# Kernel optimization log

Hardware: AMD Instinct MI355X
Metric: run time of the kernel (lower is better)

The kernel has to match this reference:

```python
import math
import jax, jax.numpy as jnp
import numpy as np

B, S, D, H, DH = 2, 2048, 2048, 16, 128  # batch, seq (= n_ctx), d_model, n_heads, d_head


def _alibi_slopes(n):
    def pow2(m):
        start = 2 ** (-2 ** (-(math.log2(m) - 3)))
        return [start * start ** i for i in range(m)]
    if math.log2(n).is_integer():
        return pow2(n)
    c = 2 ** math.floor(math.log2(n))
    return pow2(c) + _alibi_slopes(2 * c)[0::2][: n - c]


def _alibi_mask(n_heads, q_len, kv_len):
    # faithful to _gen_alibi_mask: causal -inf upper triangle + slope * key_position
    slopes = jnp.asarray(np.array(_alibi_slopes(n_heads), dtype=np.float32))  # [H]
    bias = slopes[:, None, None] * jnp.arange(kv_len, dtype=jnp.float32)[None, None, :]  # [H,1,kv]
    i = jnp.arange(q_len)[:, None]
    j = jnp.arange(kv_len)[None, :]
    causal = jnp.where(j > i, -jnp.inf, 0.0).astype(jnp.float32)  # [q,kv] (q_len == kv_len here)
    return causal[None, :, :] + bias  # [H,q,kv]


def setup_inputs() -> dict:
    key = jax.random.key(0)
    k1, k2, k3, k4, k5 = jax.random.split(key, 5)
    scale = 1.0 / math.sqrt(D)
    return {
        "resid_pre": jax.random.normal(k1, (B, S, D), dtype=jnp.float32),
        "Wq": jax.random.normal(k2, (H * DH, D), dtype=jnp.float32) * scale,
        "Wk": jax.random.normal(k3, (H * DH, D), dtype=jnp.float32) * scale,
        "Wv": jax.random.normal(k4, (H * DH, D), dtype=jnp.float32) * scale,
        "Wo": jax.random.normal(k5, (D, H * DH), dtype=jnp.float32) * scale,
    }


def reference(resid_pre, Wq, Wk, Wv, Wo):
    b, s, d = resid_pre.shape
    # nn.Linear(no bias): y = x @ W^T ; view to [b, s, H, DH]
    q = (resid_pre @ Wq.T).reshape(b, s, H, DH)
    k = (resid_pre @ Wk.T).reshape(b, s, H, DH)
    v = (resid_pre @ Wv.T).reshape(b, s, H, DH)
    # QK^T / sqrt(d_head), clamp, add ALiBi+causal mask
    scores = jnp.einsum('bqhd,bkhd->bhqk', q, k) / math.sqrt(DH)
    scores = jnp.clip(scores, -1024.0, 1024.0)
    scores = scores + _alibi_mask(H, s, s)[None]  # broadcast over batch
    attn = jax.nn.softmax(scores.astype(jnp.float32), axis=-1).astype(q.dtype)
    z = jnp.einsum('bhqk,bkhd->bqhd', attn, v)  # [b,s,H,DH]
    # out_proj.weight [D, H*DH] reshaped to [D, H, DH]; per-head out summed over heads
    out = jnp.einsum('bqhd,ohd->bqo', z, Wo.reshape(d, H, DH))
    return out
```

## Files before the change

kernel.cpp:

```cpp
#include <hip/hip_runtime.h>
#include <hip/hip_bf16.h>

typedef __attribute__((ext_vector_type(4))) float f32x4;
typedef __attribute__((ext_vector_type(8))) short bf16x8;
typedef __attribute__((ext_vector_type(4))) short short4v;

__device__ __forceinline__ short f2bf(float f) {
  union { float f; unsigned u; } x; x.f = f;
  unsigned r = x.u + 0x7fffu + ((x.u >> 16) & 1u);
  return (short)(r >> 16);
}

__device__ __forceinline__ float fexp2(float x) {
#if __has_builtin(__builtin_amdgcn_exp2f)
  return __builtin_amdgcn_exp2f(x);
#else
  return exp2f(x);
#endif
}

#define WAITVM4() { asm volatile("s_waitcnt vmcnt(4)" ::: "memory"); __builtin_amdgcn_sched_barrier(0); }
#define BARRIER() { __builtin_amdgcn_sched_barrier(0); asm volatile("s_barrier" ::: "memory"); __builtin_amdgcn_sched_barrier(0); }
#define GLD16(g, l) __builtin_amdgcn_global_load_lds((const __attribute__((address_space(1))) void*)(g), (__attribute__((address_space(3))) void*)(l), 16, 0, 0)

__global__ __launch_bounds__(256) void cast_kernel(const float* __restrict__ in,
                                                   short* __restrict__ out, int n4) {
  int i = blockIdx.x * 256 + threadIdx.x;
  if (i < n4) {
    const float4 v = reinterpret_cast<const float4*>(in)[i];
    short4v s;
    s.x = f2bf(v.x); s.y = f2bf(v.y); s.z = f2bf(v.z); s.w = f2bf(v.w);
    reinterpret_cast<short4v*>(out)[i] = s;
  }
}

__global__ __launch_bounds__(256) void cast_w_kernel(const float* __restrict__ w0,
                                                     const float* __restrict__ w1,
                                                     const float* __restrict__ w2,
                                                     const float* __restrict__ w3,
                                                     short* __restrict__ qkv,
                                                     short* __restrict__ wo) {
  const int y = blockIdx.y;
  const float* in = (y == 0) ? w0 : (y == 1) ? w1 : (y == 2) ? w2 : w3;
  short* out = (y < 3) ? (qkv + (long)y * 4194304) : wo;
  const int i = blockIdx.x * 256 + threadIdx.x;
  const float4 v = reinterpret_cast<const float4*>(in)[i];
  short4v s;
  s.x = f2bf(v.x); s.y = f2bf(v.y); s.z = f2bf(v.z); s.w = f2bf(v.w);
  reinterpret_cast<short4v*>(out)[i] = s;
}

__global__ __launch_bounds__(512, 2) void gemm_qkv8(const short* __restrict__ A,
                                                    const short* __restrict__ W,
                                                    short* __restrict__ Qo,
                                                    short* __restrict__ Ko,
                                                    short* __restrict__ Vt) {
  __shared__ __align__(1024) char lds[131072];
  const int tid  = threadIdx.x;
  const int lane = tid & 63;
  const int w    = tid >> 6;
  const int wm   = w >> 2, wn = w & 3;
  const int l16  = lane & 15, g = lane >> 4;
  const int K    = 2048;

  int id = (int)blockIdx.x;
  id = (id & 7) * 48 + (id >> 3);
  const int mb = id & 15, nb = id >> 4;
  const long m0 = (long)mb * 256, n0 = (long)nb * 256;

  const int srow = lane >> 3;
  const int scol = ((lane & 7) ^ srow) * 8;
  const int csw  = (l16 & 7) << 4;

  f32x4 acc[8][4];
  #pragma unroll
  for (int a = 0; a < 8; a++)
    #pragma unroll
    for (int b = 0; b < 4; b++) acc[a][b] = (f32x4){0.f, 0.f, 0.f, 0.f};

  #define STAGE_HALF(mat, rbase, h, kt, buf, isB)                                   \
    {                                                                               \
      const long rowg = (rbase) + (h) * 128 + w * 16 + srow;                        \
      const short* s0_ = (mat) + rowg * K + (kt) * 64 + scol;                       \
      char* d_ = lds + (buf) * 65536 + (isB) * 32768 + ((h) * 128 + w * 16) * 128;  \
      GLD16(s0_, d_);                                                               \
      GLD16(s0_ + 8LL * K, d_ + 1024);                                              \
    }

  #define RDA(buf, h, fmL, k) (*reinterpret_cast<const bf16x8*>(                    \
      lds + (buf) * 65536 + (((h) * 128 + wm * 64 + (fmL) * 16 + l16) * 128) +      \
      (((k) * 64 + g * 16) ^ csw)))
  #define RDB(buf, h, fnL, k) (*reinterpret_cast<const bf16x8*>(                    \
      lds + (buf) * 65536 + 32768 + (((h) * 128 + wn * 32 + (fnL) * 16 + l16) * 128) + \
      (((k) * 64 + g * 16) ^ csw)))

  STAGE_HALF(A, m0, 0, 0, 0, 0);
  STAGE_HALF(W, n0, 0, 0, 0, 1);
  STAGE_HALF(W, n0, 1, 0, 0, 1);
  STAGE_HALF(A, m0, 1, 0, 0, 0);
  WAITVM4();
  BARRIER();

  bf16x8 af[4][2], bfr[2][2];
  for (int kt = 0; kt < 32; ++kt) {
    const int cur = kt & 1, nxt = cur ^ 1;
    const int ks = (kt + 1 < 32) ? (kt + 1) : kt;

    #pragma unroll
    for (int fm = 0; fm < 4; fm++)
      #pragma unroll
      for (int k = 0; k < 2; k++) af[fm][k] = RDA(cur, 0, fm, k);
    #pragma unroll
    for (int j = 0; j < 2; j++)
      #pragma unroll
      for (int k = 0; k < 2; k++) bfr[j][k] = RDB(cur, 0, j, k);
    STAGE_HALF(A, m0, 0, ks, nxt, 0);
    WAITVM4();
    BARRIER();
    __builtin_amdgcn_s_setprio(1);
    #pragma unroll
    for (int fm = 0; fm < 4; fm++)
      #pragma unroll
      for (int j = 0; j < 2; j++)
        #pragma unroll
        for (int k = 0; k < 2; k++)
          acc[fm][j] = __builtin_amdgcn_mfma_f32_16x16x32_bf16(af[fm][k], bfr[j][k], acc[fm][j], 0, 0, 0);
    __builtin_amdgcn_s_setprio(0);
    BARRIER();

    #pragma unroll
    for (int j = 0; j < 2; j++)
      #pragma unroll
      for (int k = 0; k < 2; k++) bfr[j][k] = RDB(cur, 1, j, k);
    STAGE_HALF(W, n0, 0, ks, nxt, 1);
    WAITVM4();
    BARRIER();
    __builtin_amdgcn_s_setprio(1);
    #pragma unroll
    for (int fm = 0; fm < 4; fm++)
      #pragma unroll
      for (int j = 0; j < 2; j++)
        #pragma unroll
        for (int k = 0; k < 2; k++)
          acc[fm][2 + j] = __builtin_amdgcn_mfma_f32_16x16x32_bf16(af[fm][k], bfr[j][k], acc[fm][2 + j], 0, 0, 0);
    __builtin_amdgcn_s_setprio(0);
    BARRIER();

    #pragma unroll
    for (int fm = 0; fm < 4; fm++)
      #pragma unroll
      for (int k = 0; k < 2; k++) af[fm][k] = RDA(cur, 1, fm, k);
    STAGE_HALF(W, n0, 1, ks, nxt, 1);
    WAITVM4();
    BARRIER();
    __builtin_amdgcn_s_setprio(1);
    #pragma unroll
    for (int fm = 0; fm < 4; fm++)
      #pragma unroll
      for (int j = 0; j < 2; j++)
        #pragma unroll
        for (int k = 0; k < 2; k++)
          acc[4 + fm][2 + j] = __builtin_amdgcn_mfma_f32_16x16x32_bf16(af[fm][k], bfr[j][k], acc[4 + fm][2 + j], 0, 0, 0);
    __builtin_amdgcn_s_setprio(0);
    BARRIER();

    #pragma unroll
    for (int j = 0; j < 2; j++)
      #pragma unroll
      for (int k = 0; k < 2; k++) bfr[j][k] = RDB(cur, 0, j, k);
    STAGE_HALF(A, m0, 1, ks, nxt, 0);
    WAITVM4();
    BARRIER();
    __builtin_amdgcn_s_setprio(1);
    #pragma unroll
    for (int fm = 0; fm < 4; fm++)
      #pragma unroll
      for (int j = 0; j < 2; j++)
        #pragma unroll
        for (int k = 0; k < 2; k++)
          acc[4 + fm][j] = __builtin_amdgcn_mfma_f32_16x16x32_bf16(af[fm][k], bfr[j][k], acc[4 + fm][j], 0, 0, 0);
    __builtin_amdgcn_s_setprio(0);
    BARRIER();
  }

  const int sect = (int)(n0 >> 11);
  #pragma unroll
  for (int fm = 0; fm < 8; fm++)
    #pragma unroll
    for (int fn = 0; fn < 4; fn++) {
      const long row0 = m0 + (fm >> 2) * 128 + wm * 64 + (fm & 3) * 16 + g * 4;
      const long col  = n0 + (fn >> 1) * 128 + wn * 32 + (fn & 1) * 16 + l16;
      if (sect == 0) {
        #pragma unroll
        for (int i = 0; i < 4; i++) Qo[(row0 + i) * 2048 + col] = f2bf(acc[fm][fn][i]);
      } else if (sect == 1) {
        #pragma unroll
        for (int i = 0; i < 4; i++) Ko[(row0 + i) * 2048 + (col - 2048)] = f2bf(acc[fm][fn][i]);
      } else {
        const long c2 = col - 4096;
        const long base = (((row0 >> 11) * 16 + (c2 >> 7)) * 128 + (c2 & 127)) * 2048 + (row0 & 2047);
        short4v pk;
        #pragma unroll
        for (int i = 0; i < 4; i++) pk[i] = f2bf(acc[fm][fn][i]);
        *reinterpret_cast<short4v*>(Vt + base) = pk;
      }
    }
  #undef STAGE_HALF
  #undef RDA
  #undef RDB
}

template<typename CT, bool TV>
__global__ __launch_bounds__(256) void gemm_bt(const short* __restrict__ A,
                                               const short* __restrict__ B,
                                               CT* __restrict__ C,
                                               int M, int N, int K) {
  __shared__ short As[128][72];
  __shared__ short Bs[128][72];

  const int tid  = threadIdx.x;
  const int lane = tid & 63;
  const int w    = tid >> 6;
  const int l16  = lane & 15, g = lane >> 4;
  const int wr   = w >> 1, wc = w & 1;
  const long m0  = (long)blockIdx.y * 128;
  const long n0  = (long)blockIdx.x * 128;

  const f32x4 zero4 = {0.f, 0.f, 0.f, 0.f};
  f32x4 acc[4][4];
  #pragma unroll
  for (int a = 0; a < 4; a++)
    #pragma unroll
    for (int b2 = 0; b2 < 4; b2++) acc[a][b2] = zero4;

  const int srow0 = tid >> 3;
  const int scol  = (tid & 7) * 8;

  const int ktiles = K >> 6;
  for (int kt = 0; kt < ktiles; kt++) {
    const int k0 = kt << 6;
    __syncthreads();
    #pragma unroll
    for (int j = 0; j < 4; j++) {
      const int row = j * 32 + srow0;
      *reinterpret_cast<bf16x8*>(&As[row][scol]) =
          *reinterpret_cast<const bf16x8*>(A + (m0 + row) * K + k0 + scol);
      *reinterpret_cast<bf16x8*>(&Bs[row][scol]) =
          *reinterpret_cast<const bf16x8*>(B + (n0 + row) * K + k0 + scol);
    }
    __syncthreads();
    #pragma unroll
    for (int kk = 0; kk < 2; kk++) {
      bf16x8 af[4], bfr[4];
      #pragma unroll
      for (int f = 0; f < 4; f++)
        af[f] = *reinterpret_cast<const bf16x8*>(&As[wr * 64 + f * 16 + l16][kk * 32 + g * 8]);
      #pragma unroll
      for (int f = 0; f < 4; f++)
        bfr[f] = *reinterpret_cast<const bf16x8*>(&Bs[wc * 64 + f * 16 + l16][kk * 32 + g * 8]);
      #pragma unroll
      for (int fm = 0; fm < 4; fm++)
        #pragma unroll
        for (int fn = 0; fn < 4; fn++)
          acc[fm][fn] = __builtin_amdgcn_mfma_f32_16x16x32_bf16(af[fm], bfr[fn], acc[fm][fn], 0, 0, 0);
    }
  }

  #pragma unroll
  for (int fm = 0; fm < 4; fm++)
    #pragma unroll
    for (int fn = 0; fn < 4; fn++) {
      const long row0 = m0 + wr * 64 + fm * 16 + g * 4;
      const long col  = n0 + wc * 64 + fn * 16 + l16;
      if constexpr (TV) {
        const long base = (((row0 >> 11) * 16 + (col >> 7)) * 128 + (col & 127)) * 2048 + (row0 & 2047);
        short4v pk;
        #pragma unroll
        for (int i = 0; i < 4; i++) pk[i] = f2bf(acc[fm][fn][i]);
        *reinterpret_cast<short4v*>(C + base) = pk;
      } else {
        #pragma unroll
        for (int i = 0; i < 4; i++) {
          const float v = acc[fm][fn][i];
          if constexpr (sizeof(CT) == 2) C[(row0 + i) * N + col] = (CT)f2bf(v);
          else                           C[(row0 + i) * N + col] = v;
        }
      }
    }
}

__global__ __launch_bounds__(256, 3) void attn_kernel(const short* __restrict__ Q,
                                                      const short* __restrict__ K,
                                                      const short* __restrict__ Vt,
                                                      short* __restrict__ Z) {
  __shared__ short Ks[64][136];
  __shared__ short Vs[128][72];
  __shared__ short plds[4][16][72];

  const int tid  = threadIdx.x;
  const int lane = tid & 63;
  const int w    = tid >> 6;
  const int l16  = lane & 15, g = lane >> 4;

  const int bh = blockIdx.x;
  const int bx = 31 - (int)blockIdx.y;
  const int b  = bh >> 4, h = bh & 15;
  const int q0 = bx * 64;

  const float LOG2E  = 1.4426950408889634f;
  const float slope2 = exp2f(-0.5f * (float)(h + 1)) * LOG2E;
  const float scale2 = 0.08838834764831845f * LOG2E;
  const float CLAMP2 = 1477.3197f;

  bf16x8 qf[4];
  {
    const long qoff = ((long)(b * 2048 + q0 + w * 16 + l16)) * 2048 + h * 128;
    #pragma unroll
    for (int c = 0; c < 4; c++)
      qf[c] = *reinterpret_cast<const bf16x8*>(Q + qoff + c * 32 + g * 8);
  }

  const f32x4 zero4 = {0.f, 0.f, 0.f, 0.f};
  f32x4 zacc[8];
  #pragma unroll
  for (int s = 0; s < 8; s++) zacc[s] = zero4;
  float m2[4], li[4];
  #pragma unroll
  for (int i = 0; i < 4; i++) { m2[i] = -3e38f; li[i] = 0.f; }

  float aj[4];
  #pragma unroll
  for (int ni = 0; ni < 4; ni++) aj[ni] = slope2 * (float)(ni * 16 + l16);

  const int krow = tid >> 4, kcol = (tid & 15) * 8;
  const int vrow = tid >> 3, vcol = (tid & 7) * 8;
  const short* Kh = K + ((long)b * 2048) * 2048 + h * 128;
  const short* Vh = Vt + ((long)(b * 16 + h) * 128) * 2048;

  bf16x8 kreg[4], vreg[4];
  #pragma unroll
  for (int j = 0; j < 4; j++)
    kreg[j] = *reinterpret_cast<const bf16x8*>(Kh + (long)(j * 16 + krow) * 2048 + kcol);
  #pragma unroll
  for (int j = 0; j < 4; j++)
    vreg[j] = *reinterpret_cast<const bf16x8*>(Vh + (long)(j * 32 + vrow) * 2048 + vcol);

  const int ntiles = bx + 1;
  for (int t = 0; t < ntiles; t++) {
    const int kv0 = t * 64;
    __syncthreads();
    #pragma unroll
    for (int j = 0; j < 4; j++)
      *reinterpret_cast<bf16x8*>(&Ks[j * 16 + krow][kcol]) = kreg[j];
    #pragma unroll
    for (int j = 0; j < 4; j++)
      *reinterpret_cast<bf16x8*>(&Vs[j * 32 + vrow][vcol]) = vreg[j];
    __syncthreads();

    f32x4 sc[4];
    #pragma unroll
    for (int ni = 0; ni < 4; ni++) sc[ni] = zero4;
    #pragma unroll
    for (int ni = 0; ni < 4; ni++)
      #pragma unroll
      for (int kc = 0; kc < 4; kc++) {
        const bf16x8 kf = *reinterpret_cast<const bf16x8*>(&Ks[ni * 16 + l16][kc * 32 + g * 8]);
        sc[ni] = __builtin_amdgcn_mfma_f32_16x16x32_bf16(qf[kc], kf, sc[ni], 0, 0, 0);
      }

    if (t + 1 < ntiles) {
      const short* kb = Kh + (long)(kv0 + 64) * 2048;
      const short* vb = Vh + kv0 + 64;
      #pragma unroll
      for (int j = 0; j < 4; j++)
        kreg[j] = *reinterpret_cast<const bf16x8*>(kb + (long)(j * 16 + krow) * 2048 + kcol);
      #pragma unroll
      for (int j = 0; j < 4; j++)
        vreg[j] = *reinterpret_cast<const bf16x8*>(vb + (long)(j * 32 + vrow) * 2048 + vcol);
    }

    const float bk = slope2 * (float)kv0;
    float best[4];
    int need = 0;
    #pragma unroll
    for (int i = 0; i < 4; i++) {
      const int qi = q0 + w * 16 + g * 4 + i;
      float bb = -3e38f;
      #pragma unroll
      for (int ni = 0; ni < 4; ni++) {
        const int j = kv0 + ni * 16 + l16;
        float v = sc[ni][i] * scale2;
        v = fminf(fmaxf(v, -CLAMP2), CLAMP2) + (bk + aj[ni]);
        v = (j <= qi) ? v : -3e38f;
        sc[ni][i] = v;
        bb = fmaxf(bb, v);
      }
      #pragma unroll
      for (int ms = 1; ms < 16; ms <<= 1) bb = fmaxf(bb, __shfl_xor(bb, ms));
      best[i] = bb;
      need |= (bb > m2[i] + 10.f) ? 1 : 0;
    }
    if (__any(need)) {
      #pragma unroll
      for (int i = 0; i < 4; i++) {
        const float mnew = fmaxf(m2[i], best[i]);
        const float corr = fexp2(m2[i] - mnew);
        m2[i] = mnew;
        li[i] *= corr;
        #pragma unroll
        for (int s = 0; s < 8; s++) zacc[s][i] *= corr;
      }
    }
    #pragma unroll
    for (int i = 0; i < 4; i++) {
      float psum = 0.f;
      #pragma unroll
      for (int ni = 0; ni < 4; ni++) {
        const float p = fexp2(sc[ni][i] - m2[i]);
        plds[w][g * 4 + i][ni * 16 + l16] = f2bf(p);
        psum += p;
      }
      li[i] += psum;
    }

    bf16x8 paf[2];
    #pragma unroll
    for (int kk = 0; kk < 2; kk++)
      paf[kk] = *reinterpret_cast<const bf16x8*>(&plds[w][l16][kk * 32 + g * 8]);
    #pragma unroll
    for (int s = 0; s < 8; s++) {
      const bf16x8 vf0 = *reinterpret_cast<const bf16x8*>(&Vs[s * 16 + l16][g * 8]);
      const bf16x8 vf1 = *reinterpret_cast<const bf16x8*>(&Vs[s * 16 + l16][32 + g * 8]);
      zacc[s] = __builtin_amdgcn_mfma_f32_16x16x32_bf16(paf[0], vf0, zacc[s], 0, 0, 0);
      zacc[s] = __builtin_amdgcn_mfma_f32_16x16x32_bf16(paf[1], vf1, zacc[s], 0, 0, 0);
    }
  }

  #pragma unroll
  for (int i = 0; i < 4; i++) {
    float s = li[i];
    #pragma unroll
    for (int ms = 1; ms < 16; ms <<= 1) s += __shfl_xor(s, ms);
    li[i] = s;
  }
  #pragma unroll
  for (int s = 0; s < 8; s++)
    #pragma unroll
    for (int i = 0; i < 4; i++) {
      const int qi = q0 + w * 16 + g * 4 + i;
      const float zv = zacc[s][i] / li[i];
      Z[((long)(b * 2048 + qi)) * 2048 + h * 128 + s * 16 + l16] = f2bf(zv);
    }
}

extern "C" void kernel_launch(void* const* d_in, const int* in_sizes, int n_in,
                              void* d_out, int out_size, void* d_ws, size_t ws_size,
                              hipStream_t stream) {
  const float* X  = (const float*)d_in[0];
  const float* Wq = (const float*)d_in[1];
  const float* Wk = (const float*)d_in[2];
  const float* Wv = (const float*)d_in[3];
  const float* Wo = (const float*)d_in[4];
  float* out = (float*)d_out;

  short* ws    = (short*)d_ws;
  short* Xb    = ws;
  short* Wqkvb = ws + 8388608;
  short* Wob   = ws + 20971520;
  short* Qb    = ws + 25165824;
  short* Kb    = ws + 33554432;
  short* Vtb   = ws + 41943040;
  short* Zb    = Xb;

  cast_kernel<<<8192, 256, 0, stream>>>(X, Xb, 2097152);
  dim3 gw(4096, 4);
  cast_w_kernel<<<gw, 256, 0, stream>>>(Wq, Wk, Wv, Wo, Wqkvb, Wob);

  gemm_qkv8<<<384, 512, 0, stream>>>(Xb, Wqkvb, Qb, Kb, Vtb);

  dim3 ga(32, 32);
  attn_kernel<<<ga, 256, 0, stream>>>(Qb, Kb, Vtb, Zb);

  dim3 gg(16, 32);
  gemm_bt<float, false><<<gg, 256, 0, stream>>>(Zb, Wob, out, 4096, 2048, 2048);
}
```

Before: 268.2 us.

## Retile QKV GEMM to 128x384 blocks with 512 workgroups

The fused QKV projection GEMM moves from 256x256 tiles (384 blocks) to 128x384 tiles (512 blocks). The K-loop is rewritten with one A stage and three B stages per iteration, new vmcnt waits, and a per-column epilogue that routes each column to Q, K or transposed V. The goal is better balance across the 256 CUs, since 384 blocks leave a partial second wave. The cost is lower arithmetic intensity per tile (more global and LDS traffic per FLOP) and LDS buffers that are now only partly used.

```diff
diff --git a/kernel.cpp b/kernel.cpp
--- a/kernel.cpp
+++ b/kernel.cpp
@@ -19,7 +19,7 @@
 #endif
 }
 
-#define WAITVM4() { asm volatile("s_waitcnt vmcnt(4)" ::: "memory"); __builtin_amdgcn_sched_barrier(0); }
+#define WAITVM(n) { asm volatile("s_waitcnt vmcnt(" #n ")" ::: "memory"); __builtin_amdgcn_sched_barrier(0); }
 #define BARRIER() { __builtin_amdgcn_sched_barrier(0); asm volatile("s_barrier" ::: "memory"); __builtin_amdgcn_sched_barrier(0); }
 #define GLD16(g, l) __builtin_amdgcn_global_load_lds((const __attribute__((address_space(1))) void*)(g), (__attribute__((address_space(3))) void*)(l), 16, 0, 0)
 
@@ -64,41 +64,47 @@
   const int K    = 2048;
 
   int id = (int)blockIdx.x;
-  id = (id & 7) * 48 + (id >> 3);
-  const int mb = id & 15, nb = id >> 4;
-  const long m0 = (long)mb * 256, n0 = (long)nb * 256;
+  id = (id & 7) * 64 + (id >> 3);
+  const int mb = id & 31, nb = id >> 5;
+  const long m0 = (long)mb * 128, n0 = (long)nb * 384;
 
   const int srow = lane >> 3;
   const int scol = ((lane & 7) ^ srow) * 8;
   const int csw  = (l16 & 7) << 4;
 
-  f32x4 acc[8][4];
-  #pragma unroll
-  for (int a = 0; a < 8; a++)
-    #pragma unroll
-    for (int b = 0; b < 4; b++) acc[a][b] = (f32x4){0.f, 0.f, 0.f, 0.f};
-
-  #define STAGE_HALF(mat, rbase, h, kt, buf, isB)                                   \
+  f32x4 acc[4][6];
+  #pragma unroll
+  for (int a = 0; a < 4; a++)
+    #pragma unroll
+    for (int b = 0; b < 6; b++) acc[a][b] = (f32x4){0.f, 0.f, 0.f, 0.f};
+
+  #define STAGE_A(kt, buf)                                                          \
     {                                                                               \
-      const long rowg = (rbase) + (h) * 128 + w * 16 + srow;                        \
-      const short* s0_ = (mat) + rowg * K + (kt) * 64 + scol;                       \
-      char* d_ = lds + (buf) * 65536 + (isB) * 32768 + ((h) * 128 + w * 16) * 128;  \
+      const short* s0_ = A + (m0 + w * 16 + srow) * K + (kt) * 64 + scol;           \
+      char* d_ = lds + (buf) * 65536 + (w * 16) * 128;                              \
       GLD16(s0_, d_);                                                               \
       GLD16(s0_ + 8LL * K, d_ + 1024);                                              \
     }
-
-  #define RDA(buf, h, fmL, k) (*reinterpret_cast<const bf16x8*>(                    \
-      lds + (buf) * 65536 + (((h) * 128 + wm * 64 + (fmL) * 16 + l16) * 128) +      \
-      (((k) * 64 + g * 16) ^ csw)))
-  #define RDB(buf, h, fnL, k) (*reinterpret_cast<const bf16x8*>(                    \
-      lds + (buf) * 65536 + 32768 + (((h) * 128 + wn * 32 + (fnL) * 16 + l16) * 128) + \
-      (((k) * 64 + g * 16) ^ csw)))
-
-  STAGE_HALF(A, m0, 0, 0, 0, 0);
-  STAGE_HALF(W, n0, 0, 0, 0, 1);
-  STAGE_HALF(W, n0, 1, 0, 0, 1);
-  STAGE_HALF(A, m0, 1, 0, 0, 0);
-  WAITVM4();
+  #define STAGE_B(h, kt, buf)                                                       \
+    {                                                                               \
+      const short* s0_ = W + (n0 + (h) * 128 + w * 16 + srow) * K + (kt) * 64 + scol; \
+      char* d_ = lds + (buf) * 65536 + 16384 + (h) * 16384 + (w * 16) * 128;        \
+      GLD16(s0_, d_);                                                               \
+      GLD16(s0_ + 8LL * K, d_ + 1024);                                              \
+    }
+
+  #define RDA(buf, fmL, k) (*reinterpret_cast<const bf16x8*>(                       \
+      lds + (buf) * 65536 + ((wm * 64 + (fmL) * 16 + l16) * 128) +                  \
+      ((((k) * 64 + g * 16)) ^ csw)))
+  #define RDB(buf, h, j, k) (*reinterpret_cast<const bf16x8*>(                      \
+      lds + (buf) * 65536 + 16384 + (h) * 16384 +                                   \
+      ((wn * 16 + (j) * 64 + l16) * 128) + ((((k) * 64 + g * 16)) ^ csw)))
+
+  STAGE_A(0, 0);
+  STAGE_B(0, 0, 0);
+  STAGE_B(1, 0, 0);
+  STAGE_B(2, 0, 0);
+  WAITVM(4);
   BARRIER();
 
   bf16x8 af[4][2], bfr[2][2];
@@ -109,13 +115,14 @@
     #pragma unroll
     for (int fm = 0; fm < 4; fm++)
       #pragma unroll
-      for (int k = 0; k < 2; k++) af[fm][k] = RDA(cur, 0, fm, k);
+      for (int k = 0; k < 2; k++) af[fm][k] = RDA(cur, fm, k);
     #pragma unroll
     for (int j = 0; j < 2; j++)
       #pragma unroll
       for (int k = 0; k < 2; k++) bfr[j][k] = RDB(cur, 0, j, k);
-    STAGE_HALF(A, m0, 0, ks, nxt, 0);
-    WAITVM4();
+    STAGE_A(ks, nxt);
+    STAGE_B(0, ks, nxt);
+    WAITVM(6);
     BARRIER();
     __builtin_amdgcn_s_setprio(1);
     #pragma unroll
@@ -132,8 +139,8 @@
     for (int j = 0; j < 2; j++)
       #pragma unroll
       for (int k = 0; k < 2; k++) bfr[j][k] = RDB(cur, 1, j, k);
-    STAGE_HALF(W, n0, 0, ks, nxt, 1);
-    WAITVM4();
+    STAGE_B(1, ks, nxt);
+    WAITVM(6);
     BARRIER();
     __builtin_amdgcn_s_setprio(1);
     #pragma unroll
@@ -147,65 +154,47 @@
     BARRIER();
 
     #pragma unroll
+    for (int j = 0; j < 2; j++)
+      #pragma unroll
+      for (int k = 0; k < 2; k++) bfr[j][k] = RDB(cur, 2, j, k);
+    STAGE_B(2, ks, nxt);
+    WAITVM(4);
+    BARRIER();
+    __builtin_amdgcn_s_setprio(1);
+    #pragma unroll
     for (int fm = 0; fm < 4; fm++)
       #pragma unroll
-      for (int k = 0; k < 2; k++) af[fm][k] = RDA(cur, 1, fm, k);
-    STAGE_HALF(W, n0, 1, ks, nxt, 1);
-    WAITVM4();
-    BARRIER();
-    __builtin_amdgcn_s_setprio(1);
-    #pragma unroll
-    for (int fm = 0; fm < 4; fm++)
-      #pragma unroll
       for (int j = 0; j < 2; j++)
         #pragma unroll
         for (int k = 0; k < 2; k++)
-          acc[4 + fm][2 + j] = __builtin_amdgcn_mfma_f32_16x16x32_bf16(af[fm][k], bfr[j][k], acc[4 + fm][2 + j], 0, 0, 0);
+          acc[fm][4 + j] = __builtin_amdgcn_mfma_f32_16x16x32_bf16(af[fm][k], bfr[j][k], acc[fm][4 + j], 0, 0, 0);
     __builtin_amdgcn_s_setprio(0);
     BARRIER();
-
-    #pragma unroll
-    for (int j = 0; j < 2; j++)
-      #pragma unroll
-      for (int k = 0; k < 2; k++) bfr[j][k] = RDB(cur, 0, j, k);
-    STAGE_HALF(A, m0, 1, ks, nxt, 0);
-    WAITVM4();
-    BARRIER();
-    __builtin_amdgcn_s_setprio(1);
-    #pragma unroll
-    for (int fm = 0; fm < 4; fm++)
-      #pragma unroll
-      for (int j = 0; j < 2; j++)
-        #pragma unroll
-        for (int k = 0; k < 2; k++)
-          acc[4 + fm][j] = __builtin_amdgcn_mfma_f32_16x16x32_bf16(af[fm][k], bfr[j][k], acc[4 + fm][j], 0, 0, 0);
-    __builtin_amdgcn_s_setprio(0);
-    BARRIER();
-  }
-
-  const int sect = (int)(n0 >> 11);
-  #pragma unroll
-  for (int fm = 0; fm < 8; fm++)
-    #pragma unroll
-    for (int fn = 0; fn < 4; fn++) {
-      const long row0 = m0 + (fm >> 2) * 128 + wm * 64 + (fm & 3) * 16 + g * 4;
-      const long col  = n0 + (fn >> 1) * 128 + wn * 32 + (fn & 1) * 16 + l16;
-      if (sect == 0) {
-        #pragma unroll
-        for (int i = 0; i < 4; i++) Qo[(row0 + i) * 2048 + col] = f2bf(acc[fm][fn][i]);
-      } else if (sect == 1) {
-        #pragma unroll
-        for (int i = 0; i < 4; i++) Ko[(row0 + i) * 2048 + (col - 2048)] = f2bf(acc[fm][fn][i]);
+  }
+
+  #pragma unroll
+  for (int fm = 0; fm < 4; fm++)
+    #pragma unroll
+    for (int fj = 0; fj < 6; fj++) {
+      const long row0 = m0 + wm * 64 + fm * 16 + g * 4;
+      const long col  = n0 + fj * 64 + wn * 16 + l16;
+      if (col < 2048) {
+        #pragma unroll
+        for (int i = 0; i < 4; i++) Qo[(row0 + i) * 2048 + col] = f2bf(acc[fm][fj][i]);
+      } else if (col < 4096) {
+        #pragma unroll
+        for (int i = 0; i < 4; i++) Ko[(row0 + i) * 2048 + (col - 2048)] = f2bf(acc[fm][fj][i]);
       } else {
         const long c2 = col - 4096;
         const long base = (((row0 >> 11) * 16 + (c2 >> 7)) * 128 + (c2 & 127)) * 2048 + (row0 & 2047);
         short4v pk;
         #pragma unroll
-        for (int i = 0; i < 4; i++) pk[i] = f2bf(acc[fm][fn][i]);
+        for (int i = 0; i < 4; i++) pk[i] = f2bf(acc[fm][fj][i]);
         *reinterpret_cast<short4v*>(Vt + base) = pk;
       }
     }
-  #undef STAGE_HALF
+  #undef STAGE_A
+  #undef STAGE_B
   #undef RDA
   #undef RDB
 }
@@ -476,7 +465,7 @@
   dim3 gw(4096, 4);
   cast_w_kernel<<<gw, 256, 0, stream>>>(Wq, Wk, Wv, Wo, Wqkvb, Wob);
 
-  gemm_qkv8<<<384, 512, 0, stream>>>(Xb, Wqkvb, Qb, Kb, Vtb);
+  gemm_qkv8<<<512, 512, 0, stream>>>(Xb, Wqkvb, Qb, Kb, Vtb);
 
   dim3 ga(32, 32);
   attn_kernel<<<ga, 256, 0, stream>>>(Qb, Kb, Vtb, Zb);
```

Result: faster. 252.6 us (-5.8%).
